# Optimization experiments

Hardware: AMD Instinct MI355X
Metric: run time of the kernel (lower is better)

The kernel has to match this reference:

```python
import jax, jax.numpy as jnp
import numpy as np

H, D = 16, 64  # num_head, num_out
LN_EPS = 1e-5

def setup_inputs() -> dict:
    key = jax.random.key(0)
    ks = jax.random.split(key, 6)
    B, S, C = 4, 2048, 1024
    sc = 0.02
    return {
        "x": jax.random.normal(ks[0], (B, S, C), jnp.float32),
        "mask": jax.random.randint(ks[1], (B, S), 0, 2, jnp.int32),
        "Wq": jax.random.normal(ks[2], (C, C), jnp.float32) * sc,
        "Wk": jax.random.normal(ks[3], (C, C), jnp.float32) * sc,
        "Wv": jax.random.normal(ks[4], (C, C), jnp.float32) * sc,
        "Wr": jax.random.normal(ks[5], (C, C), jnp.float32) * sc,
        "gamma": jnp.ones((C,), jnp.float32),
        "beta": jnp.zeros((C,), jnpip := jnp.float32) if False else jnp.zeros((C,), jnp.float32),
    }

def reference(x, mask, Wq, Wk, Wv, Wr, gamma, beta):
    B, S, C = x.shape
    # torch Linear: y = x @ W.T ; split(num_out,-1) == reshape (B,S,H,D)
    q = (x @ Wq.T).reshape(B, S, H, D)
    k = (x @ Wk.T).reshape(B, S, H, D)
    v = (x @ Wv.T).reshape(B, S, H, D)
    scores = jnp.einsum("bqhd,bkhd->bhqk", q, k) / jnp.sqrt(jnp.float32(D))
    # mask [B,S] over keys; masked positions -> -1e9 (matches masked_fill)
    scores = jnp.where((mask == 0)[:, None, None, :], jnp.float32(-1e9), scores)
    attn = jax.nn.softmax(scores, axis=-1)
    out = jnp.einsum("bhqk,bkhd->bqhd", attn, v).reshape(B, S, H * D)
    out = jax.nn.relu(out + x @ Wr.T)
    mu = jnp.mean(out, axis=-1, keepdims=True)
    var = jnp.mean(jnp.square(out - mu), axis=-1, keepdims=True)
    return (out - mu) / jnp.sqrt(var + LN_EPS) * gamma + beta
```

## Files before the change

### kernel.cpp

```cpp
#include <hip/hip_runtime.h>

typedef __attribute__((ext_vector_type(8))) short short8;
typedef __attribute__((ext_vector_type(8))) unsigned short u16x8;
typedef __attribute__((ext_vector_type(4))) float f32x4;
typedef __attribute__((ext_vector_type(4))) unsigned short u16x4;
typedef __attribute__((ext_vector_type(4))) float float4v;

#define MFMA(a, b, c) __builtin_amdgcn_mfma_f32_16x16x32_bf16(a, b, c, 0, 0, 0)
#define GLOAD_LDS16(gp, lp) __builtin_amdgcn_global_load_lds( \
    (const __attribute__((address_space(1))) void*)(gp),      \
    (__attribute__((address_space(3))) void*)(lp), 16, 0, 0)

__device__ __forceinline__ float bf2f(unsigned short u) {
    union { unsigned int i; float f; } v; v.i = ((unsigned int)u) << 16; return v.f;
}
__device__ __forceinline__ unsigned short f2bf(float f) {
    union { float f; unsigned int i; } v; v.f = f;
    unsigned int r = (v.i + 0x7FFFu + ((v.i >> 16) & 1u)) >> 16;
    return (unsigned short)r;
}
__device__ __forceinline__ unsigned short f2bfr(float f) {
    union { float f; unsigned int i; } v; v.f = f;
    return (unsigned short)((v.i + 0x8000u) >> 16);
}

__global__ __launch_bounds__(256)
void mask_scan(const int* __restrict__ mask, int* __restrict__ kidx, int* __restrict__ seff)
{
    constexpr int S = 2048;
    const int b = blockIdx.x;
    const int tid = threadIdx.x;
    __shared__ int ps[256];
    const int* m = mask + b * S;
    int loc[8], s = 0;
#pragma unroll
    for (int j = 0; j < 8; ++j) { loc[j] = m[tid * 8 + j]; s += loc[j]; }
#pragma unroll
    for (int j = 0; j < 8; ++j) kidx[b * S + tid * 8 + j] = b * S;
    ps[tid] = s;
    __syncthreads();
    for (int off = 1; off < 256; off <<= 1) {
        int v = (tid >= off) ? ps[tid - off] : 0;
        __syncthreads();
        ps[tid] += v;
        __syncthreads();
    }
    int run = (tid > 0) ? ps[tid - 1] : 0;
#pragma unroll
    for (int j = 0; j < 8; ++j) {
        if (loc[j]) kidx[b * S + run] = b * S + tid * 8 + j;
        run += loc[j];
    }
    if (tid == 255) seff[b] = ps[255];
}

__global__ __launch_bounds__(256)
void ingest_all(const float* __restrict__ X,
                const float* __restrict__ Wq, const float* __restrict__ Wk,
                const float* __restrict__ Wv, const float* __restrict__ Wr,
                unsigned short* __restrict__ dst)
{
    constexpr int X4 = 2097152;
    constexpr int T4 = X4 + 4 * 262144;
    const int stride = gridDim.x * blockDim.x;
    for (int i = blockIdx.x * blockDim.x + threadIdx.x; i < T4; i += stride) {
        const float* src;
        int off;
        if (i < X4) { src = X; off = i; }
        else {
            int jj = i - X4;
            int ws = jj >> 18;
            off = jj & 0x3FFFF;
            src = (ws == 0) ? Wq : (ws == 1) ? Wk : (ws == 2) ? Wv : Wr;
        }
        float4v v = ((const float4v*)src)[off];
        u16x4 o;
#pragma unroll
        for (int j = 0; j < 4; ++j) o[j] = f2bf(v[j]);
        ((u16x4*)dst)[i] = o;
    }
}

__global__ __launch_bounds__(256)
void proj_gemm(const unsigned short* __restrict__ X,
               const unsigned short* __restrict__ Wq, const unsigned short* __restrict__ Wk,
               const unsigned short* __restrict__ Wv, const unsigned short* __restrict__ Wr,
               unsigned short* __restrict__ Qo, unsigned short* __restrict__ Ko,
               unsigned short* __restrict__ Vo, unsigned short* __restrict__ Ro,
               const int* __restrict__ kidx, const int* __restrict__ seff)
{
    constexpr int Kd = 1024, N = 1024;
    __shared__ unsigned short smem[128 * 136];
    unsigned short* As = smem;
    unsigned short* Bs = smem + 8192;
    unsigned short* Ct = smem;
    const int tid = threadIdx.x;
    const int wid = tid >> 6, lane = tid & 63;
    const int g = lane >> 4, lr = lane & 15;
    const int bid = blockIdx.x;
    const int jx = bid & 7, t = bid >> 3;
    const int x = (t >> 5) * 8 + jx;
    const int c = t & 31;
    const int wsel = c >> 3;
    const int coltile = c & 7;
    const bool compact = (wsel == 1) || (wsel == 2);
    int rowBase;
    if (compact) {
        if (x >= 68) return;
        int b = x / 17, xt = x - b * 17;
        if (xt * 128 >= seff[b]) return;
        rowBase = b * 2048 + xt * 128;
    } else {
        if (x >= 64) return;
        rowBase = x * 128;
    }
    const unsigned short* W = (wsel == 0) ? Wq : (wsel == 1) ? Wk : (wsel == 2) ? Wv : Wr;
    unsigned short* O = (wsel == 0) ? Qo : (wsel == 1) ? Ko : (wsel == 2) ? Vo : Ro;
    const int colBase = coltile * 128;
    const int wm = wid >> 1, wn = wid & 1;

    f32x4 acc[4][4] = {};

    const unsigned short* srcA[4];
    const unsigned short* srcB[4];
#pragma unroll
    for (int i = 0; i < 4; ++i) {
        int n = tid + 256 * i;
        int r = n >> 3;
        int cb = (n & 7) ^ (r & 7);
        int sA = compact ? kidx[rowBase + r] : rowBase + r;
        srcA[i] = X + (size_t)sA * Kd + cb * 8;
        srcB[i] = W + (size_t)(colBase + r) * Kd + cb * 8;
    }

    for (int kt = 0; kt < Kd; kt += 64) {
        if (kt) __syncthreads();
#pragma unroll
        for (int i = 0; i < 4; ++i)
            GLOAD_LDS16(srcA[i] + kt, As + (size_t)(tid + 256 * i) * 8);
#pragma unroll
        for (int i = 0; i < 4; ++i)
            GLOAD_LDS16(srcB[i] + kt, Bs + (size_t)(tid + 256 * i) * 8);
        asm volatile("s_waitcnt vmcnt(0)" ::: "memory");
        __syncthreads();
#pragma unroll
        for (int kkb = 0; kkb < 8; kkb += 4) {
            short8 a[4], b[4];
#pragma unroll
            for (int mt = 0; mt < 4; ++mt) {
                int row = wm * 64 + mt * 16 + lr;
                a[mt] = *reinterpret_cast<const short8*>(
                    &As[row * 64 + (((g + kkb) ^ (lr & 7)) << 3)]);
            }
#pragma unroll
            for (int nt = 0; nt < 4; ++nt) {
                int row = wn * 64 + nt * 16 + lr;
                b[nt] = *reinterpret_cast<const short8*>(
                    &Bs[row * 64 + (((g + kkb) ^ (lr & 7)) << 3)]);
            }
#pragma unroll
            for (int mt = 0; mt < 4; ++mt)
#pragma unroll
                for (int nt = 0; nt < 4; ++nt)
                    acc[mt][nt] = MFMA(a[mt], b[nt], acc[mt][nt]);
        }
    }
    __syncthreads();
#pragma unroll
    for (int mt = 0; mt < 4; ++mt)
#pragma unroll
        for (int nt = 0; nt < 4; ++nt)
#pragma unroll
            for (int r = 0; r < 4; ++r)
                Ct[(wm * 64 + mt * 16 + g * 4 + r) * 136 + wn * 64 + nt * 16 + lr] =
                    f2bf(acc[mt][nt][r]);
    __syncthreads();
#pragma unroll
    for (int pp = 0; pp < 8; ++pp) {
        int row = pp * 16 + (tid >> 4);
        int col = (tid & 15) * 8;
        u16x8 v8 = *reinterpret_cast<const u16x8*>(&Ct[row * 136 + col]);
        *reinterpret_cast<u16x8*>(&O[(size_t)(rowBase + row) * N + colBase + col]) = v8;
    }
}

__global__ __launch_bounds__(512)
void attn_fwd(const unsigned short* __restrict__ Q, const unsigned short* __restrict__ Kb,
              const unsigned short* __restrict__ Vb, const int* __restrict__ seff,
              unsigned short* __restrict__ AO)
{
    constexpr int S = 2048, C = 1024, Dh = 64;
    constexpr int PST = 64;
    constexpr float SCL = 0.125f * 1.44269504f;
    constexpr float FM  = 16.0f;
    constexpr float MSK = -1.0e30f;
    __shared__ unsigned short Kt[2][64 * 64];
    __shared__ unsigned short Vt[2][64 * 64];
    __shared__ unsigned short Pt[8][16 * PST];
    const int tid = threadIdx.x;
    const int w = tid >> 6, lane = tid & 63;
    const int g = lane >> 4, lr = lane & 15;
    const int lin = blockIdx.x;
    const int hb = lin & 63, qt = lin >> 6;
    const int h = hb >> 2, b = hb & 3;
    const int qbase = qt * 128;
    const int qrow = qbase + w * 16 + lr;

    const int Sb = seff[b];
    const int ntiles = (Sb + 63) >> 6;

    const unsigned short* qptr = Q + (size_t)(b * S + qrow) * C + h * Dh;
    short8 qf[2];
    qf[0] = *reinterpret_cast<const short8*>(qptr + g * 8);
    qf[1] = *reinterpret_cast<const short8*>(qptr + 32 + g * 8);

    short8 ones;
#pragma unroll
    for (int j = 0; j < 8; ++j) ones[j] = (short)0x3F80;

    f32x4 o[4] = {};
    f32x4 lacc = {};

    const unsigned short* kg = Kb + (size_t)(b * S) * C + h * Dh;
    const unsigned short* vg = Vb + (size_t)(b * S) * C + h * Dh;

    const int kk0 = tid >> 3;
    const int kd0 = ((tid & 7) ^ (kk0 & 7)) * 8;
    const int vkey = tid >> 3;
    const int vsd = (tid & 7) * 8;

    short8 vv;
    GLOAD_LDS16(kg + (size_t)kk0 * C + kd0, &Kt[0][(size_t)tid * 8]);
    vv = *reinterpret_cast<const short8*>(vg + (size_t)vkey * C + vsd);
    asm volatile("s_waitcnt vmcnt(0)" ::: "memory");
    {
        const unsigned short* bb = (const unsigned short*)&vv;
#pragma unroll
        for (int j = 0; j < 8; ++j) {
            int d = vsd + j;
            int sw = (d & 7) ^ ((d >> 3) & 7);
            Vt[0][d * 64 + ((((vkey >> 3) ^ sw) << 3) | (vkey & 7))] = bb[j];
        }
    }
    __syncthreads();

    int cur = 0;
    for (int tt = 0; tt < ntiles; ++tt) {
        const int t = tt * 64;
        const bool hasNext = (tt + 1) < ntiles;
        if (hasNext) {
            const int tn = t + 64;
            GLOAD_LDS16(kg + (size_t)(tn + kk0) * C + kd0, &Kt[cur ^ 1][(size_t)tid * 8]);
            vv = *reinterpret_cast<const short8*>(vg + (size_t)(tn + vkey) * C + vsd);
        }
        f32x4 s[4];
        __builtin_amdgcn_s_setprio(1);
#pragma unroll
        for (int nt = 0; nt < 4; ++nt) {
            int key = nt * 16 + lr;
            f32x4 a = {};
#pragma unroll
            for (int c = 0; c < 2; ++c) {
                int dd = c * 32 + g * 8;
                short8 kf = *reinterpret_cast<const short8*>(
                    &Kt[cur][key * 64 + (((dd >> 3) ^ (key & 7)) << 3)]);
                a = MFMA(qf[c], kf, a);
            }
            s[nt] = a;
        }
        __builtin_amdgcn_s_setprio(0);
        float madd[4];
#pragma unroll
        for (int nt = 0; nt < 4; ++nt)
            madd[nt] = ((t + nt * 16 + lr) < Sb) ? -FM : MSK;
        unsigned short* Pw = Pt[w];
#pragma unroll
        for (int nt = 0; nt < 4; ++nt) {
            int k = nt * 16 + lr;
#pragma unroll
            for (int r = 0; r < 4; ++r) {
                float p = __builtin_amdgcn_exp2f(s[nt][r] * SCL + madd[nt]);
                int row = g * 4 + r;
                Pw[row * PST + ((((k >> 3) ^ (row & 7)) << 3) | (k & 7))] = f2bfr(p);
            }
        }
        asm volatile("s_waitcnt lgkmcnt(0)" ::: "memory");
        __builtin_amdgcn_sched_barrier(0);
        short8 pf[2];
#pragma unroll
        for (int hh = 0; hh < 2; ++hh) {
            int kk = hh * 32 + g * 8;
            pf[hh] = *reinterpret_cast<const short8*>(
                &Pw[lr * PST + (((kk >> 3) ^ (lr & 7)) << 3)]);
        }
        __builtin_amdgcn_s_setprio(1);
        lacc = MFMA(pf[0], ones, lacc);
        lacc = MFMA(pf[1], ones, lacc);
#pragma unroll
        for (int dt = 0; dt < 4; ++dt) {
            int d = dt * 16 + lr;
#pragma unroll
            for (int hh = 0; hh < 2; ++hh) {
                int kk = hh * 32 + g * 8;
                short8 vf = *reinterpret_cast<const short8*>(
                    &Vt[cur][d * 64 + ((((kk >> 3) ^ (d & 7) ^ ((d >> 3) & 7)) << 3))]);
                o[dt] = MFMA(pf[hh], vf, o[dt]);
            }
        }
        __builtin_amdgcn_s_setprio(0);
        if (hasNext) {
            asm volatile("s_waitcnt vmcnt(0)" ::: "memory");
            const unsigned short* bb = (const unsigned short*)&vv;
            unsigned short* Vn = Vt[cur ^ 1];
#pragma unroll
            for (int j = 0; j < 8; ++j) {
                int d = vsd + j;
                int sw = (d & 7) ^ ((d >> 3) & 7);
                Vn[d * 64 + ((((vkey >> 3) ^ sw) << 3) | (vkey & 7))] = bb[j];
            }
        }
        __syncthreads();
        cur ^= 1;
    }
#pragma unroll
    for (int dt = 0; dt < 4; ++dt)
#pragma unroll
        for (int r = 0; r < 4; ++r) {
            int row = qbase + w * 16 + g * 4 + r;
            int col = h * Dh + dt * 16 + lr;
            AO[(size_t)(b * S + row) * C + col] = f2bf(o[dt][r] / lacc[r]);
        }
}

__global__ __launch_bounds__(256)
void ln_ep(const unsigned short* __restrict__ AO, const unsigned short* __restrict__ R,
           const float* __restrict__ gamma, const float* __restrict__ beta,
           float* __restrict__ out)
{
    constexpr int C = 1024;
    const int row = blockIdx.x;
    const int tid = threadIdx.x;
    __shared__ float red[4][2];

    float v[4]; float sum = 0.f, ss = 0.f;
    u16x4 av = *reinterpret_cast<const u16x4*>(AO + (size_t)row * C + tid * 4);
    u16x4 rv = *reinterpret_cast<const u16x4*>(R + (size_t)row * C + tid * 4);
#pragma unroll
    for (int i = 0; i < 4; ++i) {
        v[i] = fmaxf(0.f, bf2f(av[i]) + bf2f(rv[i]));
        sum += v[i]; ss += v[i] * v[i];
    }
#pragma unroll
    for (int off = 1; off < 64; off <<= 1) {
        sum += __shfl_xor(sum, off, 64);
        ss += __shfl_xor(ss, off, 64);
    }
    int w = tid >> 6;
    if ((tid & 63) == 0) { red[w][0] = sum; red[w][1] = ss; }
    __syncthreads();
    sum = red[0][0] + red[1][0] + red[2][0] + red[3][0];
    ss = red[0][1] + red[1][1] + red[2][1] + red[3][1];
    float mu = sum * (1.f / C);
    float var = ss * (1.f / C) - mu * mu;
    float rstd = rsqrtf(var + 1e-5f);
    float4v g4 = *reinterpret_cast<const float4v*>(gamma + tid * 4);
    float4v b4 = *reinterpret_cast<const float4v*>(beta + tid * 4);
    float4v ov;
#pragma unroll
    for (int i = 0; i < 4; ++i)
        ov[i] = (v[i] - mu) * rstd * g4[i] + b4[i];
    *reinterpret_cast<float4v*>(out + (size_t)row * C + tid * 4) = ov;
}

extern "C" void kernel_launch(void* const* d_in, const int* in_sizes, int n_in,
                              void* d_out, int out_size, void* d_ws, size_t ws_size,
                              hipStream_t stream)
{
    const float* X = (const float*)d_in[0];
    const int* mask = (const int*)d_in[1];
    const float* Wq = (const float*)d_in[2];
    const float* Wk = (const float*)d_in[3];
    const float* Wv = (const float*)d_in[4];
    const float* Wr = (const float*)d_in[5];
    const float* Gm = (const float*)d_in[6];
    const float* Bt = (const float*)d_in[7];
    float* out = (float*)d_out;

    const size_t NE = (size_t)8192 * 1024;
    const size_t WE = (size_t)1024 * 1024;
    unsigned short* p = (unsigned short*)d_ws;
    unsigned short* Xb = p;   p += NE;
    unsigned short* Wqb = p;  p += WE;
    unsigned short* Wkb = p;  p += WE;
    unsigned short* Wvb = p;  p += WE;
    unsigned short* Wrb = p;  p += WE;
    unsigned short* Qb = p;   p += NE;
    unsigned short* Kb = p;   p += NE;
    unsigned short* Vb = p;   p += NE;
    unsigned short* Rb = p;   p += NE;
    int* kidx = (int*)p;      p += 8192 * 2;
    int* seff = (int*)p;      p += 8;
    unsigned short* AO = Xb;

    mask_scan<<<dim3(4), 256, 0, stream>>>(mask, kidx, seff);
    ingest_all<<<dim3(2048), 256, 0, stream>>>(X, Wq, Wk, Wv, Wr, Xb);

    proj_gemm<<<dim3(2304), 256, 0, stream>>>(Xb, Wqb, Wkb, Wvb, Wrb,
                                              Qb, Kb, Vb, Rb, kidx, seff);
    attn_fwd<<<dim3(1024), 512, 0, stream>>>(Qb, Kb, Vb, seff, AO);
    ln_ep<<<dim3(8192), 256, 0, stream>>>(AO, Rb, Gm, Bt, out);
}
```

Measured before the change: 165.1 us.

## Write V transposed from projection GEMM and load it directly into LDS

The projection GEMM now writes V in a per-batch transposed layout [B][C][S] through a transposed LDS staging step. The attention kernel can then fill its V tile with direct global-to-LDS loads, the same way it loads K. This removes the per-thread register load plus eight scalar scattered LDS writes per tile and simplifies the swizzle. The cost is a transposed epilogue in the GEMM, only for the V tiles, which changes the LDS write pattern there.

```diff
diff --git a/kernel.cpp b/kernel.cpp
--- a/kernel.cpp
+++ b/kernel.cpp
@@ -86,7 +86,7 @@
                const unsigned short* __restrict__ Wq, const unsigned short* __restrict__ Wk,
                const unsigned short* __restrict__ Wv, const unsigned short* __restrict__ Wr,
                unsigned short* __restrict__ Qo, unsigned short* __restrict__ Ko,
-               unsigned short* __restrict__ Vo, unsigned short* __restrict__ Ro,
+               unsigned short* __restrict__ VT, unsigned short* __restrict__ Ro,
                const int* __restrict__ kidx, const int* __restrict__ seff)
 {
     constexpr int Kd = 1024, N = 1024;
@@ -115,7 +115,7 @@
         rowBase = x * 128;
     }
     const unsigned short* W = (wsel == 0) ? Wq : (wsel == 1) ? Wk : (wsel == 2) ? Wv : Wr;
-    unsigned short* O = (wsel == 0) ? Qo : (wsel == 1) ? Ko : (wsel == 2) ? Vo : Ro;
+    unsigned short* O = (wsel == 0) ? Qo : (wsel == 1) ? Ko : (wsel == 2) ? VT : Ro;
     const int colBase = coltile * 128;
     const int wm = wid >> 1, wn = wid & 1;
 
@@ -166,27 +166,49 @@
         }
     }
     __syncthreads();
-#pragma unroll
-    for (int mt = 0; mt < 4; ++mt)
-#pragma unroll
-        for (int nt = 0; nt < 4; ++nt)
-#pragma unroll
-            for (int r = 0; r < 4; ++r)
-                Ct[(wm * 64 + mt * 16 + g * 4 + r) * 136 + wn * 64 + nt * 16 + lr] =
-                    f2bf(acc[mt][nt][r]);
-    __syncthreads();
-#pragma unroll
-    for (int pp = 0; pp < 8; ++pp) {
-        int row = pp * 16 + (tid >> 4);
-        int col = (tid & 15) * 8;
-        u16x8 v8 = *reinterpret_cast<const u16x8*>(&Ct[row * 136 + col]);
-        *reinterpret_cast<u16x8*>(&O[(size_t)(rowBase + row) * N + colBase + col]) = v8;
+    if (wsel == 2) {
+#pragma unroll
+        for (int mt = 0; mt < 4; ++mt)
+#pragma unroll
+            for (int nt = 0; nt < 4; ++nt)
+#pragma unroll
+                for (int r = 0; r < 4; ++r)
+                    Ct[(wn * 64 + nt * 16 + lr) * 136 + wm * 64 + mt * 16 + g * 4 + r] =
+                        f2bf(acc[mt][nt][r]);
+        __syncthreads();
+        const int bq = rowBase >> 11;
+        const int tok0 = rowBase & 2047;
+#pragma unroll
+        for (int pp = 0; pp < 8; ++pp) {
+            int colf = pp * 16 + (tid >> 4);
+            int tkb = (tid & 15) * 8;
+            u16x8 v8 = *reinterpret_cast<const u16x8*>(&Ct[colf * 136 + tkb]);
+            *reinterpret_cast<u16x8*>(
+                &O[(size_t)bq * 2097152 + (size_t)(colBase + colf) * 2048 + tok0 + tkb]) = v8;
+        }
+    } else {
+#pragma unroll
+        for (int mt = 0; mt < 4; ++mt)
+#pragma unroll
+            for (int nt = 0; nt < 4; ++nt)
+#pragma unroll
+                for (int r = 0; r < 4; ++r)
+                    Ct[(wm * 64 + mt * 16 + g * 4 + r) * 136 + wn * 64 + nt * 16 + lr] =
+                        f2bf(acc[mt][nt][r]);
+        __syncthreads();
+#pragma unroll
+        for (int pp = 0; pp < 8; ++pp) {
+            int row = pp * 16 + (tid >> 4);
+            int col = (tid & 15) * 8;
+            u16x8 v8 = *reinterpret_cast<const u16x8*>(&Ct[row * 136 + col]);
+            *reinterpret_cast<u16x8*>(&O[(size_t)(rowBase + row) * N + colBase + col]) = v8;
+        }
     }
 }
 
 __global__ __launch_bounds__(512)
 void attn_fwd(const unsigned short* __restrict__ Q, const unsigned short* __restrict__ Kb,
-              const unsigned short* __restrict__ Vb, const int* __restrict__ seff,
+              const unsigned short* __restrict__ VT, const int* __restrict__ seff,
               unsigned short* __restrict__ AO)
 {
     constexpr int S = 2048, C = 1024, Dh = 64;
@@ -222,26 +244,16 @@
     f32x4 lacc = {};
 
     const unsigned short* kg = Kb + (size_t)(b * S) * C + h * Dh;
-    const unsigned short* vg = Vb + (size_t)(b * S) * C + h * Dh;
+    const unsigned short* vtg = VT + (size_t)b * 2097152 + (size_t)(h * Dh) * 2048;
 
     const int kk0 = tid >> 3;
     const int kd0 = ((tid & 7) ^ (kk0 & 7)) * 8;
-    const int vkey = tid >> 3;
-    const int vsd = (tid & 7) * 8;
-
-    short8 vv;
+    const int vd = tid >> 3;
+    const int vkb = ((tid & 7) ^ (vd & 7)) * 8;
+
     GLOAD_LDS16(kg + (size_t)kk0 * C + kd0, &Kt[0][(size_t)tid * 8]);
-    vv = *reinterpret_cast<const short8*>(vg + (size_t)vkey * C + vsd);
+    GLOAD_LDS16(vtg + (size_t)vd * 2048 + vkb, &Vt[0][(size_t)tid * 8]);
     asm volatile("s_waitcnt vmcnt(0)" ::: "memory");
-    {
-        const unsigned short* bb = (const unsigned short*)&vv;
-#pragma unroll
-        for (int j = 0; j < 8; ++j) {
-            int d = vsd + j;
-            int sw = (d & 7) ^ ((d >> 3) & 7);
-            Vt[0][d * 64 + ((((vkey >> 3) ^ sw) << 3) | (vkey & 7))] = bb[j];
-        }
-    }
     __syncthreads();
 
     int cur = 0;
@@ -251,7 +263,7 @@
         if (hasNext) {
             const int tn = t + 64;
             GLOAD_LDS16(kg + (size_t)(tn + kk0) * C + kd0, &Kt[cur ^ 1][(size_t)tid * 8]);
-            vv = *reinterpret_cast<const short8*>(vg + (size_t)(tn + vkey) * C + vsd);
+            GLOAD_LDS16(vtg + (size_t)vd * 2048 + tn + vkb, &Vt[cur ^ 1][(size_t)tid * 8]);
         }
         f32x4 s[4];
         __builtin_amdgcn_s_setprio(1);
@@ -303,22 +315,12 @@
             for (int hh = 0; hh < 2; ++hh) {
                 int kk = hh * 32 + g * 8;
                 short8 vf = *reinterpret_cast<const short8*>(
-                    &Vt[cur][d * 64 + ((((kk >> 3) ^ (d & 7) ^ ((d >> 3) & 7)) << 3))]);
+                    &Vt[cur][d * 64 + ((((kk >> 3) ^ (d & 7)) << 3))]);
                 o[dt] = MFMA(pf[hh], vf, o[dt]);
             }
         }
         __builtin_amdgcn_s_setprio(0);
-        if (hasNext) {
-            asm volatile("s_waitcnt vmcnt(0)" ::: "memory");
-            const unsigned short* bb = (const unsigned short*)&vv;
-            unsigned short* Vn = Vt[cur ^ 1];
-#pragma unroll
-            for (int j = 0; j < 8; ++j) {
-                int d = vsd + j;
-                int sw = (d & 7) ^ ((d >> 3) & 7);
-                Vn[d * 64 + ((((vkey >> 3) ^ sw) << 3) | (vkey & 7))] = bb[j];
-            }
-        }
+        if (hasNext) asm volatile("s_waitcnt vmcnt(0)" ::: "memory");
         __syncthreads();
         cur ^= 1;
     }
@@ -396,7 +398,7 @@
     unsigned short* Wrb = p;  p += WE;
     unsigned short* Qb = p;   p += NE;
     unsigned short* Kb = p;   p += NE;
-    unsigned short* Vb = p;   p += NE;
+    unsigned short* VTb = p;  p += NE;
     unsigned short* Rb = p;   p += NE;
     int* kidx = (int*)p;      p += 8192 * 2;
     int* seff = (int*)p;      p += 8;
@@ -406,7 +408,7 @@
     ingest_all<<<dim3(2048), 256, 0, stream>>>(X, Wq, Wk, Wv, Wr, Xb);
 
     proj_gemm<<<dim3(2304), 256, 0, stream>>>(Xb, Wqb, Wkb, Wvb, Wrb,
-                                              Qb, Kb, Vb, Rb, kidx, seff);
-    attn_fwd<<<dim3(1024), 512, 0, stream>>>(Qb, Kb, Vb, seff, AO);
+                                              Qb, Kb, VTb, Rb, kidx, seff);
+    attn_fwd<<<dim3(1024), 512, 0, stream>>>(Qb, Kb, VTb, seff, AO);
     ln_ep<<<dim3(8192), 256, 0, stream>>>(AO, Rb, Gm, Bt, out);
 }
```

New measurement: 162.0 us. Within noise of the previous version (-1.9%).
